# Optimization experiments

Hardware: AMD Instinct MI355X
Metric: run time of the kernel (lower is better)

The kernel has to match this reference:

```python
import jax, jax.numpy as jnp
import numpy as np

ATTN_SCALE = 0.12
HEAD_DIM = 128


def _rms_norm(x):
    # F.rms_norm with no weight; eps defaults to machine eps of dtype
    eps = jnp.asarray(jnp.finfo(x.dtype).eps, x.dtype)
    return x * jax.lax.rsqrt(jnp.mean(x * x, axis=-1, keepdims=True) + eps)


def _rope(x):
    # x: [B, T, H, D]; standard rotary over (first-half, second-half) pairs
    T, D = x.shape[1], x.shape[-1]
    half = D // 2
    inv_freq = 1.0 / (10000.0 ** (jnp.arange(half, dtype=jnp.float32) / half))
    ang = jnp.arange(T, dtype=jnp.float32)[:, None] * inv_freq[None, :]  # [T, half]
    cos = jnp.cos(ang)[None, :, None, :].astype(x.dtype)
    sin = jnp.sin(ang)[None, :, None, :].astype(x.dtype)
    x1, x2 = x[..., :half], x[..., half:]
    return jnp.concatenate([x1 * cos - x2 * sin, x1 * sin + x2 * cos], axis=-1)


def setup_inputs() -> dict:
    key = jax.random.key(0)
    ks = jax.random.split(key, 4)
    B, T, dim, H, hd = 4, 2048, 1024, 8, HEAD_DIM
    hdim = H * hd
    std = 0.5 * dim ** (-0.5)
    bound = (3.0 ** 0.5) * std
    return {
        "x": jax.random.normal(ks[0], (B, T, dim), jnp.float32),
        "ve": jax.random.normal(ks[1], (B, T, hdim), jnp.float32),
        "qkv_w": jax.random.uniform(ks[2], (3, hdim, dim), jnp.float32, -bound, bound),
        "lambdas": jnp.array([0.5, 0.5], jnp.float32),
        "c_proj_w": jax.random.normal(ks[3], (dim, hdim), jnp.float32) * (hdim ** -0.5),
        "c_proj_b": jnp.zeros((dim,), jnp.float32),
    }


def reference(x, ve, qkv_w, lambdas, c_proj_w, c_proj_b):
    B, T, dim = x.shape
    hdim = qkv_w.shape[1]
    hd = HEAD_DIM
    H = hdim // hd
    # fused QKV projection: [B,T,3,H,hd]
    qkv = jnp.einsum('btd,ehd->bteh', x, qkv_w.reshape(3 * hdim, dim).reshape(3 * H, hd, dim).reshape(3 * hdim // hd, hd, dim))
    qkv = jnp.einsum('btd,fd->btf', x, qkv_w.reshape(3 * hdim, dim)).reshape(B, T, 3, H, hd)
    q, k, v = qkv[:, :, 0], qkv[:, :, 1], qkv[:, :, 2]  # each [B,T,H,hd]
    q, k = _rms_norm(q), _rms_norm(k)
    q, k = _rope(q), _rope(k)
    v = lambdas[0] * v + lambdas[1] * ve.reshape(B, T, H, hd)
    # causal SDPA with custom scale
    scores = jnp.einsum('bthd,bshd->bhts', q, k) * ATTN_SCALE  # [B,H,T,T]
    causal = jnp.tril(jnp.ones((T, T), dtype=bool))
    scores = jnp.where(causal[None, None], scores, jnp.finfo(scores.dtype).min)
    p = jax.nn.softmax(scores, axis=-1)
    y = jnp.einsum('bhts,bshd->bthd', p, v).reshape(B, T, hdim)
    return y @ c_proj_w.T + c_proj_b
```

## Files before the change

kernel.cpp:

```cpp
#include <hip/hip_runtime.h>
#include <math.h>

typedef unsigned short u16;
typedef short bf16x8 __attribute__((ext_vector_type(8)));
typedef u16 u16x2 __attribute__((ext_vector_type(2)));
typedef u16 u16x4 __attribute__((ext_vector_type(4)));
typedef u16 u16x8 __attribute__((ext_vector_type(8)));
typedef float f32x2 __attribute__((ext_vector_type(2)));
typedef float f32x4 __attribute__((ext_vector_type(4)));
typedef float f32x16 __attribute__((ext_vector_type(16)));

typedef __attribute__((address_space(1))) const void gvoid_t;
typedef __attribute__((address_space(3))) void lvoid_t;

__device__ __forceinline__ u16 f2bf(float f) {
  union { float f; unsigned u; } v; v.f = f;
  unsigned r = v.u + 0x7fffu + ((v.u >> 16) & 1u);
  return (u16)(r >> 16);
}
__device__ __forceinline__ float bf2f(u16 h) {
  union { unsigned u; float f; } v; v.u = ((unsigned)h) << 16;
  return v.f;
}
__device__ __forceinline__ f32x4 mfma16(bf16x8 a, bf16x8 b, f32x4 c) {
  return __builtin_amdgcn_mfma_f32_16x16x32_bf16(a, b, c, 0, 0, 0);
}
__device__ __forceinline__ f32x16 mfma32(bf16x8 a, bf16x8 b, f32x16 c) {
  return __builtin_amdgcn_mfma_f32_32x32x16_bf16(a, b, c, 0, 0, 0);
}
__device__ __forceinline__ void gload_lds16(const void* g, void* l) {
  __builtin_amdgcn_global_load_lds((gvoid_t*)g, (lvoid_t*)l, 16, 0, 0);
}
__device__ __forceinline__ unsigned cvtpk_bf16(float lo, float hi) {
  unsigned r;
  asm("v_cvt_pk_bf16_f32 %0, %1, %2" : "=v"(r) : "v"(lo), "v"(hi));
  return r;
}
__device__ __forceinline__ void pswap32(unsigned& a, unsigned& b) {
  asm("v_permlane32_swap_b32 %0, %1" : "+v"(a), "+v"(b));
}

#if __has_builtin(__builtin_amdgcn_exp2f)
#define EXPW(x) __builtin_amdgcn_exp2f(x)
#define SCALE_W 0.17312354f
#define DEFER_THR 11.5415603f
#else
#define EXPW(x) __expf(x)
#define SCALE_W 0.12f
#define DEFER_THR 8.0f
#endif

#define BAR() __builtin_amdgcn_s_barrier()
#define WAITLGKM()                          \
  asm volatile("s_waitcnt lgkmcnt(0)");     \
  __builtin_amdgcn_sched_barrier(0)
#define WAITVMC(N)                                    \
  do {                                                \
    __builtin_amdgcn_s_waitcnt(0x0F70 | (N));         \
    __builtin_amdgcn_sched_barrier(0);                \
  } while (0)

__global__ __launch_bounds__(256) void cvt_bf16_kernel(const float* __restrict__ in,
                                                       u16* __restrict__ out, int n4) {
  int i = blockIdx.x * 256 + threadIdx.x;
  if (i >= n4) return;
  f32x4 v = *(const f32x4*)(in + (size_t)i * 4);
  u16x4 o;
  o[0] = f2bf(v[0]); o[1] = f2bf(v[1]); o[2] = f2bf(v[2]); o[3] = f2bf(v[3]);
  *(u16x4*)(out + (size_t)i * 4) = o;
}

__global__ __launch_bounds__(256) void rope_tab_kernel(float* __restrict__ ct,
                                                       float* __restrict__ st) {
  int i = blockIdx.x * 256 + threadIdx.x;
  int t = i >> 6, j = i & 63;
  float inv = powf(10000.f, -(float)j * (1.0f / 64.0f));
  float ang = (float)t * inv;
  ct[i] = cosf(ang);
  st[i] = sinf(ang);
}

__global__ __launch_bounds__(512, 1) void gemm192_kernel(
    const u16* __restrict__ A, const u16* __restrict__ B, u16* __restrict__ C,
    int M, int N, int K, int nbn) {
  constexpr int WM = 128;
  constexpr int MI = 4;
  constexpr int NI = 3;
  constexpr int AR = 4;
  constexpr int NR = 7;
  __shared__ u16 Alds[2][256 * 64];
  __shared__ u16 Blds[2][192 * 64];
  int nwg = gridDim.x;
  int cpx = nwg >> 3;
  int bid = blockIdx.x;
  int swz = (bid & 7) * cpx + (bid >> 3);
  int bm = (swz & 3) + 4 * (swz / (4 * nbn));
  int bn = (swz >> 2) % nbn;
  size_t m0 = (size_t)bm * 256, n0 = (size_t)bn * 192;
  int tid = threadIdx.x, wid = tid >> 6, lane = tid & 63;
  int wr = wid >> 2, wc = wid & 3, l15 = lane & 15, l4 = lane >> 4;
  int srow = tid >> 3, sch = tid & 7;

  const u16* Abase = A + m0 * K;
  const u16* Bbase = B + n0 * K;

  f32x4 acc[8][NI];
#pragma unroll
  for (int m = 0; m < 8; m++)
#pragma unroll
    for (int n = 0; n < NI; n++) acc[m][n] = f32x4{0.f, 0.f, 0.f, 0.f};

  auto stageR = [&](int buf, int kt, int r) {
    if (r < AR) {
      int row = 64 * r + srow;
      gload_lds16(Abase + (size_t)row * K + kt * 64 + 8 * (sch ^ (row & 7)),
                  &Alds[buf][(64 * r + 8 * wid) * 64]);
    } else {
      int row = 64 * (r - AR) + srow;
      gload_lds16(Bbase + (size_t)row * K + kt * 64 + 8 * (sch ^ (row & 7)),
                  &Blds[buf][(64 * (r - AR) + 8 * wid) * 64]);
    }
  };
  auto rdA = [&](int buf, int half, bf16x8 (&a)[MI][2]) {
#pragma unroll
    for (int mi = 0; mi < MI; ++mi)
#pragma unroll
      for (int kk = 0; kk < 2; ++kk) {
        int row = WM * wr + 64 * half + 16 * mi + l15;
        a[mi][kk] = *(const bf16x8*)((const char*)(&Alds[buf][0]) + row * 128 +
                                     ((kk * 64 + 16 * l4) ^ ((row & 7) << 4)));
      }
  };
  auto rdB = [&](int buf, bf16x8 (&bb)[NI][2]) {
#pragma unroll
    for (int ni = 0; ni < NI; ++ni)
#pragma unroll
      for (int kk = 0; kk < 2; ++kk) {
        int row = 48 * wc + 16 * ni + l15;
        bb[ni][kk] = *(const bf16x8*)((const char*)(&Blds[buf][0]) + row * 128 +
                                      ((kk * 64 + 16 * l4) ^ ((row & 7) << 4)));
      }
  };

#define HALFM(AF, BF, QM)                                                 \
  do {                                                                    \
    __builtin_amdgcn_s_setprio(1);                                        \
    _Pragma("unroll") for (int mi = 0; mi < MI; ++mi)                     \
        _Pragma("unroll") for (int ni = 0; ni < NI; ++ni)                 \
            _Pragma("unroll") for (int kk = 0; kk < 2; ++kk)              \
                acc[4 * QM + mi][ni] =                                    \
        mfma16(AF[mi][kk], BF[ni][kk], acc[4 * QM + mi][ni]);             \
    __builtin_amdgcn_s_setprio(0);                                        \
  } while (0)

#pragma unroll
  for (int r = 0; r < NR; ++r) stageR(0, 0, r);
  WAITVMC(0);
  BAR();

  int nk = K >> 6;
  bf16x8 a[MI][2], b[NI][2];
  for (int t = 0; t < nk; ++t) {
    int buf = t & 1, nxt = buf ^ 1;
    bool pf = (t + 1 < nk);
    rdA(buf, 0, a);
    rdB(buf, b);
    if (pf) { stageR(nxt, t + 1, 0); stageR(nxt, t + 1, 1); stageR(nxt, t + 1, 2); stageR(nxt, t + 1, 3); }
    BAR();
    WAITLGKM();
    HALFM(a, b, 0);
    BAR();
    rdA(buf, 1, a);
    if (pf) { stageR(nxt, t + 1, 4); stageR(nxt, t + 1, 5); stageR(nxt, t + 1, 6); }
    BAR();
    WAITLGKM();
    HALFM(a, b, 1);
    WAITVMC(0);
    BAR();
  }

#pragma unroll
  for (int mi = 0; mi < 8; ++mi) {
#pragma unroll
    for (int ni = 0; ni < NI; ++ni) {
      size_t row = m0 + WM * wr + 16 * mi + 4 * l4;
      size_t col = n0 + 48 * wc + 16 * ni + l15;
#pragma unroll
      for (int i = 0; i < 4; ++i) {
        C[(row + i) * N + col] = f2bf(acc[mi][ni][i]);
      }
    }
  }
#undef HALFM
}

template <int BM, int OUTF32>
__global__ __launch_bounds__(512, 1) void gemm4p_kernel(
    const u16* __restrict__ A, const u16* __restrict__ B, void* __restrict__ C,
    const float* __restrict__ bias, int M, int N, int K, int nbn) {
  constexpr int WM = BM / 2;
  constexpr int MI = WM / 32;
  constexpr int NACC = 2 * MI;
  constexpr int AR = BM / 64;
  __shared__ u16 Alds[2][BM * 64];
  __shared__ u16 Blds[2][256 * 64];
  int nwg = gridDim.x;
  int cpx = nwg >> 3;
  int bid = blockIdx.x;
  int swz = (bid & 7) * cpx + (bid >> 3);
  int bm = (swz & 3) + 4 * (swz / (4 * nbn));
  int bn = (swz >> 2) % nbn;
  size_t m0 = (size_t)bm * BM, n0 = (size_t)bn * 256;
  int tid = threadIdx.x, wid = tid >> 6, lane = tid & 63;
  int wr = wid >> 2, wc = wid & 3, l15 = lane & 15, l4 = lane >> 4;
  int srow = tid >> 3, sch = tid & 7;

  const u16* Abase = A + m0 * K;
  const u16* Bbase = B + n0 * K;

  f32x4 acc[NACC][4];
#pragma unroll
  for (int m = 0; m < NACC; m++)
#pragma unroll
    for (int n = 0; n < 4; n++) acc[m][n] = f32x4{0.f, 0.f, 0.f, 0.f};

  auto stageR = [&](int buf, int kt, int r) {
    if (r < AR) {
      int row = 64 * r + srow;
      gload_lds16(Abase + (size_t)row * K + kt * 64 + 8 * (sch ^ (row & 7)),
                  &Alds[buf][(64 * r + 8 * wid) * 64]);
    } else {
      int row = 64 * (r - AR) + srow;
      gload_lds16(Bbase + (size_t)row * K + kt * 64 + 8 * (sch ^ (row & 7)),
                  &Blds[buf][(64 * (r - AR) + 8 * wid) * 64]);
    }
  };
  auto rdA = [&](int buf, int qm, bf16x8 (&a)[MI][2]) {
#pragma unroll
    for (int mi = 0; mi < MI; ++mi)
#pragma unroll
      for (int kk = 0; kk < 2; ++kk) {
        int row = WM * wr + (WM / 2) * qm + 16 * mi + l15;
        a[mi][kk] = *(const bf16x8*)((const char*)(&Alds[buf][0]) + row * 128 +
                                     ((kk * 64 + 16 * l4) ^ ((row & 7) << 4)));
      }
  };
  auto rdB = [&](int buf, int qn, bf16x8 (&bb)[2][2]) {
#pragma unroll
    for (int ni = 0; ni < 2; ++ni)
#pragma unroll
      for (int kk = 0; kk < 2; ++kk) {
        int row = 64 * wc + 32 * qn + 16 * ni + l15;
        bb[ni][kk] = *(const bf16x8*)((const char*)(&Blds[buf][0]) + row * 128 +
                                      ((kk * 64 + 16 * l4) ^ ((row & 7) << 4)));
      }
  };

#define QUADX(AF, BF, QM, QN)                                             \
  do {                                                                    \
    __builtin_amdgcn_s_setprio(1);                                        \
    _Pragma("unroll") for (int mi = 0; mi < MI; ++mi)                     \
        _Pragma("unroll") for (int ni = 0; ni < 2; ++ni)                  \
            _Pragma("unroll") for (int kk = 0; kk < 2; ++kk)              \
                acc[MI * QM + mi][2 * QN + ni] =                          \
        mfma16(AF[mi][kk], BF[ni][kk], acc[MI * QM + mi][2 * QN + ni]);   \
    __builtin_amdgcn_s_setprio(0);                                        \
  } while (0)

  constexpr int NR = AR + 4;
#pragma unroll
  for (int r = 0; r < NR; ++r) stageR(0, 0, r);
  WAITVMC(0);
  BAR();

  int nk = K >> 6;
  bf16x8 a[MI][2], b0[2][2], b1[2][2];
  for (int t = 0; t < nk; ++t) {
    int buf = t & 1, nxt = buf ^ 1;
    bool pf = (t + 1 < nk);
    rdA(buf, 0, a);
    rdB(buf, 0, b0);
    if (pf) {
      if constexpr (BM == 256) { stageR(nxt, t + 1, 0); stageR(nxt, t + 1, 1); stageR(nxt, t + 1, 2); }
      else { stageR(nxt, t + 1, 0); stageR(nxt, t + 1, 1); }
    }
    BAR();
    WAITLGKM();
    QUADX(a, b0, 0, 0);
    BAR();
    rdB(buf, 1, b1);
    if (pf) {
      if constexpr (BM == 256) { stageR(nxt, t + 1, 3); stageR(nxt, t + 1, 4); stageR(nxt, t + 1, 5); }
      else { stageR(nxt, t + 1, 2); stageR(nxt, t + 1, 3); }
    }
    BAR();
    WAITLGKM();
    QUADX(a, b1, 0, 1);
    BAR();
    rdA(buf, 1, a);
    if (pf) {
      if constexpr (BM == 256) { stageR(nxt, t + 1, 6); stageR(nxt, t + 1, 7); }
      else { stageR(nxt, t + 1, 4); stageR(nxt, t + 1, 5); }
    }
    BAR();
    WAITLGKM();
    QUADX(a, b0, 1, 0);
    BAR();
    QUADX(a, b1, 1, 1);
    WAITVMC(0);
    BAR();
  }

#pragma unroll
  for (int mi = 0; mi < NACC; ++mi) {
#pragma unroll
    for (int ni = 0; ni < 4; ++ni) {
      size_t row = m0 + WM * wr + 16 * mi + 4 * l4;
      size_t col = n0 + 64 * wc + 16 * ni + l15;
#pragma unroll
      for (int i = 0; i < 4; ++i) {
        float v = acc[mi][ni][i];
        if constexpr (OUTF32) {
          ((float*)C)[(row + i) * N + col] = v + bias[col];
        } else {
          ((u16*)C)[(row + i) * N + col] = f2bf(v);
        }
      }
    }
  }
#undef QUADX
}

__global__ __launch_bounds__(256) void transform_kernel(
    const u16* __restrict__ qkv, const float* __restrict__ ve,
    const float* __restrict__ lam, const float* __restrict__ ct,
    const float* __restrict__ st, u16* __restrict__ qn, u16* __restrict__ kn,
    u16* __restrict__ vt) {
  constexpr int T = 2048;
  __shared__ u16 vtile[64][136];
  int tt = blockIdx.x, bh = blockIdx.y;
  int b = bh >> 3, h = bh & 7;
  int tid = threadIdx.x, wid = tid >> 6, lane = tid & 63;
  int lsub = lane & 15, lrow = lane >> 4;
  float l0 = lam[0], l1 = lam[1];
  int d0 = 8 * lsub;
  float sgn = (lsub < 8) ? -1.f : 1.f;
  int jj = d0 & 63;
#pragma unroll
  for (int it = 0; it < 4; ++it) {
    int tl = wid * 16 + it * 4 + lrow;
    int t = tt * 64 + tl;
    size_t base = ((size_t)(b * T + t)) * 3072 + h * 128 + d0;
    u16x8 qraw = *(const u16x8*)(qkv + base);
    u16x8 kraw = *(const u16x8*)(qkv + base + 1024);
    u16x8 vraw = *(const u16x8*)(qkv + base + 2048);
    const float* vep = ve + ((size_t)(b * T + t)) * 1024 + h * 128 + d0;
    f32x4 ve0 = *(const f32x4*)(vep);
    f32x4 ve1 = *(const f32x4*)(vep + 4);
    float q[8], k[8];
    float sq = 0.f, sk = 0.f;
#pragma unroll
    for (int i = 0; i < 8; ++i) {
      q[i] = bf2f(qraw[i]); k[i] = bf2f(kraw[i]);
      sq += q[i] * q[i]; sk += k[i] * k[i];
    }
#pragma unroll
    for (int m = 1; m < 16; m <<= 1) {
      sq += __shfl_xor(sq, m);
      sk += __shfl_xor(sk, m);
    }
    float qs = rsqrtf(sq * (1.f / 128.f) + 1.1920929e-7f);
    float ks = rsqrtf(sk * (1.f / 128.f) + 1.1920929e-7f);
#pragma unroll
    for (int i = 0; i < 8; ++i) { q[i] *= qs; k[i] *= ks; }
    f32x4 c0 = *(const f32x4*)(ct + t * 64 + jj);
    f32x4 c1 = *(const f32x4*)(ct + t * 64 + jj + 4);
    f32x4 s0 = *(const f32x4*)(st + t * 64 + jj);
    f32x4 s1 = *(const f32x4*)(st + t * 64 + jj + 4);
    u16x8 oq, ok, ov;
#pragma unroll
    for (int i = 0; i < 8; ++i) {
      float qp = __shfl_xor(q[i], 8), kp = __shfl_xor(k[i], 8);
      float cc = (i < 4) ? c0[i & 3] : c1[i & 3];
      float ss = (i < 4) ? s0[i & 3] : s1[i & 3];
      oq[i] = f2bf(q[i] * cc + sgn * qp * ss);
      ok[i] = f2bf(k[i] * cc + sgn * kp * ss);
      float vv = (i < 4) ? ve0[i & 3] : ve1[i & 3];
      ov[i] = f2bf(l0 * bf2f(vraw[i]) + l1 * vv);
    }
    size_t orow = ((size_t)bh * T + t) * 128 + d0;
    *(u16x8*)(qn + orow) = oq;
    *(u16x8*)(kn + orow) = ok;
    *(u16x8*)&vtile[tl][d0] = ov;
  }
  __syncthreads();
#pragma unroll
  for (int it = 0; it < 4; ++it) {
    int ci = it * 256 + tid;
    int d = ci >> 3, c8 = ci & 7;
    u16x8 o;
#pragma unroll
    for (int u = 0; u < 8; u++) o[u] = vtile[c8 * 8 + u][d];
    *(u16x8*)(vt + ((size_t)bh * 128 + d) * T + tt * 64 + c8 * 8) = o;
  }
}

__global__ __launch_bounds__(256, 2) void attn_kernel(
    const u16* __restrict__ Qn, const u16* __restrict__ Kn,
    const u16* __restrict__ Vt, u16* __restrict__ Y) {
  constexpr int T = 2048;
  __shared__ u16 Klds[2][64 * 128];
  __shared__ u16 Vlds[2][128 * 64];
  int bid = blockIdx.x;
  int g = bid >> 5;
  int s = (g < 8) ? (15 - g) : (g - 8);
  int bh = bid & 31;
  int b = bh >> 3, h = bh & 7;
  int tid = threadIdx.x, wid = tid >> 6, lane = tid & 63;
  int l31 = lane & 31, hh = lane >> 5;
  const u16* Qb = Qn + (size_t)bh * T * 128;
  const u16* Kb = Kn + (size_t)bh * T * 128;
  const u16* Vb = Vt + (size_t)bh * 128 * T;
  int q0w = s * 128 + wid * 32;
  int qmaxw = q0w + 31;
  int ktend = 2 * s + 2;
  int qg = q0w + l31;

  bf16x8 qf[8];
  {
    const u16* qr = Qb + (size_t)(q0w + l31) * 128 + 8 * hh;
#pragma unroll
    for (int ks = 0; ks < 8; ks++) qf[ks] = *(const bf16x8*)(qr + 16 * ks);
  }
  f32x16 acc[4];
#pragma unroll
  for (int mt = 0; mt < 4; mt++)
#pragma unroll
    for (int r = 0; r < 16; r++) acc[mt][r] = 0.f;
  float m_run = -1e30f, l_run = 0.f;

  auto stage = [&](int buf, int kt) {
#pragma unroll
    for (int it = 0; it < 4; ++it) {
      int id = wid * 256 + it * 64 + lane;
      int r = id >> 4, c = id & 15;
      gload_lds16(Kb + (size_t)(kt * 64 + r) * 128 + 8 * (c ^ (r & 7)),
                  &Klds[buf][(size_t)(wid * 256 + it * 64) * 8]);
      int rv = id >> 3, cv = id & 7;
      gload_lds16(Vb + (size_t)rv * T + kt * 64 + 8 * (cv ^ (rv & 7)),
                  &Vlds[buf][(size_t)(wid * 256 + it * 64) * 8]);
    }
  };

  stage(0, 0);

  for (int kt = 0; kt < ktend; ++kt) {
    int cur = kt & 1;
    if (kt + 1 < ktend) {
      stage(cur ^ 1, kt + 1);
      WAITVMC(8);
    } else {
      WAITVMC(0);
    }
    BAR();
    if (kt * 64 <= qmaxw) {
      const char* kb = (const char*)&Klds[cur][0];
      const char* vb = (const char*)&Vlds[cur][0];
      int rswz = (l31 & 7) << 4;
      f32x16 st0, st1;
#pragma unroll
      for (int r = 0; r < 16; r++) { st0[r] = 0.f; st1[r] = 0.f; }
      __builtin_amdgcn_s_setprio(1);
#pragma unroll
      for (int ks = 0; ks < 8; ks++) {
        bf16x8 kf0 = *(const bf16x8*)(kb + ((l31 * 256 + 32 * ks + 16 * hh) ^ rswz));
        bf16x8 kf1 = *(const bf16x8*)(kb + (((32 + l31) * 256 + 32 * ks + 16 * hh) ^ rswz));
        st0 = mfma32(kf0, qf[ks], st0);
        st1 = mfma32(kf1, qf[ks], st1);
      }
      __builtin_amdgcn_s_setprio(0);
      bool edge = (kt == (qmaxw >> 6));
      if (edge) {
#pragma unroll
        for (int r = 0; r < 16; r++) {
          int kvb = kt * 64 + (r & 3) + 8 * (r >> 2) + 4 * hh;
          if (kvb > qg) st0[r] = -1e30f;
          if (kvb + 32 > qg) st1[r] = -1e30f;
        }
      }
      float m8[8];
#pragma unroll
      for (int r = 0; r < 8; r++)
        m8[r] = fmaxf(fmaxf(st0[r], st0[r + 8]), fmaxf(st1[r], st1[r + 8]));
#pragma unroll
      for (int r = 0; r < 4; r++) m8[r] = fmaxf(m8[r], m8[r + 4]);
      float pm = fmaxf(fmaxf(m8[0], m8[1]), fmaxf(m8[2], m8[3]));
      pm = fmaxf(pm, __shfl_xor(pm, 32));
      float pmn = pm * SCALE_W;
      bool nos = __all(pmn <= m_run + DEFER_THR);
      float mnew = nos ? m_run : fmaxf(m_run, pmn);
      if (!nos) {
        float alpha = EXPW(m_run - mnew);
        l_run *= alpha;
#pragma unroll
        for (int mt = 0; mt < 4; mt++)
#pragma unroll
          for (int r = 0; r < 16; r++) acc[mt][r] *= alpha;
        m_run = mnew;
      }
      float sa = 0.f, sb = 0.f, sc = 0.f, sd = 0.f;
#pragma unroll
      for (int r = 0; r < 4; r++) {
        st0[r]      = EXPW(fmaf(st0[r],      SCALE_W, -mnew)); sa += st0[r];
        st0[r + 4]  = EXPW(fmaf(st0[r + 4],  SCALE_W, -mnew)); sb += st0[r + 4];
        st0[r + 8]  = EXPW(fmaf(st0[r + 8],  SCALE_W, -mnew)); sc += st0[r + 8];
        st0[r + 12] = EXPW(fmaf(st0[r + 12], SCALE_W, -mnew)); sd += st0[r + 12];
        st1[r]      = EXPW(fmaf(st1[r],      SCALE_W, -mnew)); sa += st1[r];
        st1[r + 4]  = EXPW(fmaf(st1[r + 4],  SCALE_W, -mnew)); sb += st1[r + 4];
        st1[r + 8]  = EXPW(fmaf(st1[r + 8],  SCALE_W, -mnew)); sc += st1[r + 8];
        st1[r + 12] = EXPW(fmaf(st1[r + 12], SCALE_W, -mnew)); sd += st1[r + 12];
      }
      float ps = (sa + sb) + (sc + sd);
      ps += __shfl_xor(ps, 32);
      l_run += ps;
      unsigned pA0[4], pB0[4], pA1[4], pB1[4];
#pragma unroll
      for (int rr = 0; rr < 4; rr++) {
        pA0[rr] = cvtpk_bf16(st0[4 * rr], st0[4 * rr + 1]);
        pB0[rr] = cvtpk_bf16(st0[4 * rr + 2], st0[4 * rr + 3]);
        pA1[rr] = cvtpk_bf16(st1[4 * rr], st1[4 * rr + 1]);
        pB1[rr] = cvtpk_bf16(st1[4 * rr + 2], st1[4 * rr + 3]);
      }
      bf16x8 pf[4];
#pragma unroll
      for (int ks2 = 0; ks2 < 4; ks2++) {
        int k1 = ks2 & 1;
        unsigned a0, b0, a1, b1;
        if (ks2 < 2) { a0 = pA0[2 * k1]; b0 = pA0[2 * k1 + 1]; a1 = pB0[2 * k1]; b1 = pB0[2 * k1 + 1]; }
        else         { a0 = pA1[2 * k1]; b0 = pA1[2 * k1 + 1]; a1 = pB1[2 * k1]; b1 = pB1[2 * k1 + 1]; }
        pswap32(a0, b0);
        pswap32(a1, b1);
        union { unsigned w[4]; bf16x8 v; } u;
        u.w[0] = a0; u.w[1] = a1; u.w[2] = b0; u.w[3] = b1;
        pf[ks2] = u.v;
      }
      __builtin_amdgcn_s_setprio(1);
#pragma unroll
      for (int mt = 0; mt < 4; mt++) {
        int row = 32 * mt + l31;
#pragma unroll
        for (int ks2 = 0; ks2 < 4; ks2++) {
          bf16x8 vf = *(const bf16x8*)(vb + ((row * 128 + 32 * ks2 + 16 * hh) ^ rswz));
          acc[mt] = mfma32(vf, pf[ks2], acc[mt]);
        }
      }
      __builtin_amdgcn_s_setprio(0);
    }
    BAR();
  }
  float linv = 1.f / l_run;
  size_t yrow = (size_t)b * T + q0w + l31;
  u16* yp = Y + yrow * 1024 + h * 128;
#pragma unroll
  for (int mt = 0; mt < 4; mt++) {
#pragma unroll
    for (int rr = 0; rr < 4; rr++) {
      u16x4 o;
#pragma unroll
      for (int i = 0; i < 4; i++) o[i] = f2bf(acc[mt][4 * rr + i] * linv);
      *(u16x4*)(yp + 32 * mt + 8 * rr + 4 * hh) = o;
    }
  }
}

extern "C" void kernel_launch(void* const* d_in, const int* in_sizes, int n_in,
                              void* d_out, int out_size, void* d_ws, size_t ws_size,
                              hipStream_t stream) {
  (void)in_sizes; (void)n_in; (void)out_size; (void)ws_size;
  const float* x = (const float*)d_in[0];
  const float* ve = (const float*)d_in[1];
  const float* qkvw = (const float*)d_in[2];
  const float* lam = (const float*)d_in[3];
  const float* cpw = (const float*)d_in[4];
  const float* cpb = (const float*)d_in[5];
  float* out = (float*)d_out;
  char* ws = (char*)d_ws;

  u16* xb   = (u16*)(ws + 0);
  u16* wqkv = (u16*)(ws + 16777216);
  u16* wp   = (u16*)(ws + 23068672);
  u16* qkv  = (u16*)(ws + 25165824);
  u16* qn   = (u16*)(ws + 75497472);
  u16* kn   = (u16*)(ws + 92274688);
  u16* vt   = (u16*)(ws + 109051904);
  float* ctab = (float*)(ws + 125829120);
  float* stab = (float*)(ws + 126353408);
  u16* y = xb;

  rope_tab_kernel<<<512, 256, 0, stream>>>(ctab, stab);
  cvt_bf16_kernel<<<8192, 256, 0, stream>>>(x, xb, 2097152);
  cvt_bf16_kernel<<<3072, 256, 0, stream>>>(qkvw, wqkv, 786432);
  cvt_bf16_kernel<<<1024, 256, 0, stream>>>(cpw, wp, 262144);
  gemm192_kernel<<<512, 512, 0, stream>>>(xb, wqkv, qkv, 8192, 3072, 1024, 16);
  transform_kernel<<<dim3(32, 32), 256, 0, stream>>>(qkv, ve, lam, ctab, stab, qn, kn, vt);
  attn_kernel<<<512, 256, 0, stream>>>(qn, kn, vt, y);
  gemm4p_kernel<128, 1><<<256, 512, 0, stream>>>(y, wp, out, cpb, 8192, 1024, 1024, 4);
}
```

Baseline: 193.1 us.

## Split QKV GEMM K-loop into four phases with partial vmcnt waits; shrink proj tile

```diff
diff --git a/kernel.cpp b/kernel.cpp
--- a/kernel.cpp
+++ b/kernel.cpp
@@ -86,8 +86,6 @@
   constexpr int WM = 128;
   constexpr int MI = 4;
   constexpr int NI = 3;
-  constexpr int AR = 4;
-  constexpr int NR = 7;
   __shared__ u16 Alds[2][256 * 64];
   __shared__ u16 Blds[2][192 * 64];
   int nwg = gridDim.x;
@@ -111,71 +109,84 @@
     for (int n = 0; n < NI; n++) acc[m][n] = f32x4{0.f, 0.f, 0.f, 0.f};
 
   auto stageR = [&](int buf, int kt, int r) {
-    if (r < AR) {
+    if (r < 4) {
       int row = 64 * r + srow;
       gload_lds16(Abase + (size_t)row * K + kt * 64 + 8 * (sch ^ (row & 7)),
                   &Alds[buf][(64 * r + 8 * wid) * 64]);
     } else {
-      int row = 64 * (r - AR) + srow;
+      int row = 64 * (r - 4) + srow;
       gload_lds16(Bbase + (size_t)row * K + kt * 64 + 8 * (sch ^ (row & 7)),
-                  &Blds[buf][(64 * (r - AR) + 8 * wid) * 64]);
-    }
-  };
-  auto rdA = [&](int buf, int half, bf16x8 (&a)[MI][2]) {
-#pragma unroll
-    for (int mi = 0; mi < MI; ++mi)
-#pragma unroll
-      for (int kk = 0; kk < 2; ++kk) {
-        int row = WM * wr + 64 * half + 16 * mi + l15;
-        a[mi][kk] = *(const bf16x8*)((const char*)(&Alds[buf][0]) + row * 128 +
-                                     ((kk * 64 + 16 * l4) ^ ((row & 7) << 4)));
-      }
-  };
-  auto rdB = [&](int buf, bf16x8 (&bb)[NI][2]) {
-#pragma unroll
-    for (int ni = 0; ni < NI; ++ni)
-#pragma unroll
-      for (int kk = 0; kk < 2; ++kk) {
-        int row = 48 * wc + 16 * ni + l15;
-        bb[ni][kk] = *(const bf16x8*)((const char*)(&Blds[buf][0]) + row * 128 +
-                                      ((kk * 64 + 16 * l4) ^ ((row & 7) << 4)));
-      }
-  };
-
-#define HALFM(AF, BF, QM)                                                 \
+                  &Blds[buf][(64 * (r - 4) + 8 * wid) * 64]);
+    }
+  };
+  auto stageS0 = [&](int buf, int kt) {
+    stageR(buf, kt, 0); stageR(buf, kt, 2);
+    stageR(buf, kt, 4); stageR(buf, kt, 5); stageR(buf, kt, 6);
+  };
+  auto stageS1 = [&](int buf, int kt) {
+    stageR(buf, kt, 1); stageR(buf, kt, 3);
+  };
+  auto rdA = [&](int buf, int half, int kk, bf16x8 (&a)[MI]) {
+#pragma unroll
+    for (int mi = 0; mi < MI; ++mi) {
+      int row = WM * wr + 64 * half + 16 * mi + l15;
+      a[mi] = *(const bf16x8*)((const char*)(&Alds[buf][0]) + row * 128 +
+                               ((kk * 64 + 16 * l4) ^ ((row & 7) << 4)));
+    }
+  };
+  auto rdB = [&](int buf, int kk, bf16x8 (&bb)[NI]) {
+#pragma unroll
+    for (int ni = 0; ni < NI; ++ni) {
+      int row = 48 * wc + 16 * ni + l15;
+      bb[ni] = *(const bf16x8*)((const char*)(&Blds[buf][0]) + row * 128 +
+                                ((kk * 64 + 16 * l4) ^ ((row & 7) << 4)));
+    }
+  };
+
+#define PH12(AF, BF, HF)                                                  \
   do {                                                                    \
     __builtin_amdgcn_s_setprio(1);                                        \
     _Pragma("unroll") for (int mi = 0; mi < MI; ++mi)                     \
         _Pragma("unroll") for (int ni = 0; ni < NI; ++ni)                 \
-            _Pragma("unroll") for (int kk = 0; kk < 2; ++kk)              \
-                acc[4 * QM + mi][ni] =                                    \
-        mfma16(AF[mi][kk], BF[ni][kk], acc[4 * QM + mi][ni]);             \
+            acc[4 * HF + mi][ni] = mfma16(AF[mi], BF[ni], acc[4 * HF + mi][ni]); \
     __builtin_amdgcn_s_setprio(0);                                        \
   } while (0)
 
-#pragma unroll
-  for (int r = 0; r < NR; ++r) stageR(0, 0, r);
-  WAITVMC(0);
+  stageS0(0, 0);
+  stageS1(0, 0);
+  WAITVMC(2);
   BAR();
 
   int nk = K >> 6;
-  bf16x8 a[MI][2], b[NI][2];
+  bf16x8 a[MI], b0[NI], b1[NI];
   for (int t = 0; t < nk; ++t) {
     int buf = t & 1, nxt = buf ^ 1;
     bool pf = (t + 1 < nk);
-    rdA(buf, 0, a);
-    rdB(buf, b);
-    if (pf) { stageR(nxt, t + 1, 0); stageR(nxt, t + 1, 1); stageR(nxt, t + 1, 2); stageR(nxt, t + 1, 3); }
+    rdA(buf, 0, 0, a);
+    rdB(buf, 0, b0);
+    if (pf) stageS0(nxt, t + 1);
     BAR();
     WAITLGKM();
-    HALFM(a, b, 0);
-    BAR();
-    rdA(buf, 1, a);
-    if (pf) { stageR(nxt, t + 1, 4); stageR(nxt, t + 1, 5); stageR(nxt, t + 1, 6); }
+    PH12(a, b0, 0);
+    BAR();
+    rdA(buf, 0, 1, a);
+    rdB(buf, 1, b1);
     BAR();
     WAITLGKM();
-    HALFM(a, b, 1);
-    WAITVMC(0);
+    PH12(a, b1, 0);
+    if (pf) { WAITVMC(5); } else { WAITVMC(0); }
+    BAR();
+    rdA(buf, 1, 0, a);
+    if (pf) stageS1(nxt, t + 1);
+    BAR();
+    WAITLGKM();
+    PH12(a, b0, 1);
+    BAR();
+    rdA(buf, 1, 1, a);
+    BAR();
+    WAITLGKM();
+    PH12(a, b1, 1);
+    if (pf) { WAITVMC(2); } else { WAITVMC(0); }
     BAR();
   }
 
@@ -183,7 +194,7 @@
   for (int mi = 0; mi < 8; ++mi) {
 #pragma unroll
     for (int ni = 0; ni < NI; ++ni) {
-      size_t row = m0 + WM * wr + 16 * mi + 4 * l4;
+      size_t row = m0 + WM * wr + 64 * (mi >> 2) + 16 * (mi & 3) + 4 * l4;
       size_t col = n0 + 48 * wc + 16 * ni + l15;
 #pragma unroll
       for (int i = 0; i < 4; ++i) {
@@ -191,7 +202,7 @@
       }
     }
   }
-#undef HALFM
+#undef PH12
 }
 
 template <int BM, int OUTF32>
@@ -199,9 +210,10 @@
     const u16* __restrict__ A, const u16* __restrict__ B, void* __restrict__ C,
     const float* __restrict__ bias, int M, int N, int K, int nbn) {
   constexpr int WM = BM / 2;
-  constexpr int MI = WM / 32;
+  constexpr int MI = (WM / 32 > 0) ? WM / 32 : 1;
   constexpr int NACC = 2 * MI;
   constexpr int AR = BM / 64;
+  constexpr int NR = AR + 4;
   __shared__ u16 Alds[2][BM * 64];
   __shared__ u16 Blds[2][256 * 64];
   int nwg = gridDim.x;
@@ -267,7 +279,6 @@
     __builtin_amdgcn_s_setprio(0);                                        \
   } while (0)
 
-  constexpr int NR = AR + 4;
 #pragma unroll
   for (int r = 0; r < NR; ++r) stageR(0, 0, r);
   WAITVMC(0);
@@ -281,27 +292,19 @@
     rdA(buf, 0, a);
     rdB(buf, 0, b0);
     if (pf) {
-      if constexpr (BM == 256) { stageR(nxt, t + 1, 0); stageR(nxt, t + 1, 1); stageR(nxt, t + 1, 2); }
-      else { stageR(nxt, t + 1, 0); stageR(nxt, t + 1, 1); }
+#pragma unroll
+      for (int r = 0; r < NR; ++r) stageR(nxt, t + 1, r);
     }
     BAR();
     WAITLGKM();
     QUADX(a, b0, 0, 0);
     BAR();
     rdB(buf, 1, b1);
-    if (pf) {
-      if constexpr (BM == 256) { stageR(nxt, t + 1, 3); stageR(nxt, t + 1, 4); stageR(nxt, t + 1, 5); }
-      else { stageR(nxt, t + 1, 2); stageR(nxt, t + 1, 3); }
-    }
     BAR();
     WAITLGKM();
     QUADX(a, b1, 0, 1);
     BAR();
     rdA(buf, 1, a);
-    if (pf) {
-      if constexpr (BM == 256) { stageR(nxt, t + 1, 6); stageR(nxt, t + 1, 7); }
-      else { stageR(nxt, t + 1, 4); stageR(nxt, t + 1, 5); }
-    }
     BAR();
     WAITLGKM();
     QUADX(a, b0, 1, 0);
@@ -604,5 +607,5 @@
   gemm192_kernel<<<512, 512, 0, stream>>>(xb, wqkv, qkv, 8192, 3072, 1024, 16);
   transform_kernel<<<dim3(32, 32), 256, 0, stream>>>(qkv, ve, lam, ctab, stab, qn, kn, vt);
   attn_kernel<<<512, 256, 0, stream>>>(qn, kn, vt, y);
-  gemm4p_kernel<128, 1><<<256, 512, 0, stream>>>(y, wp, out, cpb, 8192, 1024, 1024, 4);
-}
+  gemm4p_kernel<64, 1><<<512, 512, 0, stream>>>(y, wp, out, cpb, 8192, 1024, 1024, 4);
+}
```

After: 195.8 us. Within noise of the previous version (+1.4%).
